# Optimization experiments

Measured on AMD Instinct MI355X. Metric: run time of the kernel, lower is better.

## Reference

```python
import jax, jax.numpy as jnp
import numpy as np

H = 4      # heads
C = 32     # out channels per head (hidden_channels)
G = 64     # num graphs


def transformer_conv(x, src, dst, Wq, bq, Wk, bk, Wv, bv, Ws, bs):
    # PyG TransformerConv, concat=False, root_weight=True, beta=False.
    N = x.shape[0]
    q = (x @ Wq + bq).reshape(N, H, C)
    k = (x @ Wk + bk).reshape(N, H, C)
    v = (x @ Wv + bv).reshape(N, H, C)
    qe = q[dst]            # [E,H,C] gather target queries
    ke = k[src]            # [E,H,C] gather source keys
    ve = v[src]            # [E,H,C] gather source values
    alpha = (qe * ke).sum(-1) / jnp.sqrt(jnp.asarray(C, x.dtype))  # [E,H]
    amax = jax.ops.segment_max(alpha, dst, num_segments=N)          # [N,H]
    a = jnp.exp(alpha - amax[dst])
    denom = jax.ops.segment_sum(a, dst, num_segments=N)             # [N,H]
    a = a / (denom[dst] + 1e-16)
    out = jax.ops.segment_sum(ve * a[..., None], dst, num_segments=N)  # [N,H,C]
    out = out.mean(axis=1)          # concat=False -> head average
    return out + x @ Ws + bs        # root skip


def setup_inputs() -> dict:
    key = jax.random.key(0)
    ks = jax.random.split(key, 24)
    N, E, Fin = 40000, 640000, 128
    x = jax.random.normal(ks[0], (N, Fin), dtype=jnp.float32)
    edge_index = jax.random.randint(ks[1], (2, E), 0, N, dtype=jnp.int64)
    batch = jnp.sort(jax.random.randint(ks[2], (N,), 0, G, dtype=jnp.int64))
    s = 0.05
    w = lambda k, shp: jax.random.normal(k, shp, dtype=jnp.float32) * s
    d = {"x": x, "edge_index": edge_index, "batch": batch,
         "Wq1": w(ks[3], (Fin, H * C)), "bq1": w(ks[4], (H * C,)),
         "Wk1": w(ks[5], (Fin, H * C)), "bk1": w(ks[6], (H * C,)),
         "Wv1": w(ks[7], (Fin, H * C)), "bv1": w(ks[8], (H * C,)),
         "Ws1": w(ks[9], (Fin, C)), "bs1": w(ks[10], (C,)),
         "Wq2": w(ks[11], (C, H * C)), "bq2": w(ks[12], (H * C,)),
         "Wk2": w(ks[13], (C, H * C)), "bk2": w(ks[14], (H * C,)),
         "Wv2": w(ks[15], (C, H * C)), "bv2": w(ks[16], (H * C,)),
         "Ws2": w(ks[17], (C, C)), "bs2": w(ks[18], (C,)),
         "Wlin": w(ks[19], (C, 16)), "blin": w(ks[20], (16,))}
    return d


def reference(x, edge_index, batch,
              Wq1, bq1, Wk1, bk1, Wv1, bv1, Ws1, bs1,
              Wq2, bq2, Wk2, bk2, Wv2, bv2, Ws2, bs2,
              Wlin, blin):
    src, dst = edge_index[0], edge_index[1]
    h = transformer_conv(x, src, dst, Wq1, bq1, Wk1, bk1, Wv1, bv1, Ws1, bs1)
    h = jax.nn.relu(h)
    h = transformer_conv(h, src, dst, Wq2, bq2, Wk2, bk2, Wv2, bv2, Ws2, bs2)
    # global mean pool over graphs
    sums = jax.ops.segment_sum(h, batch, num_segments=G)                  # [G,C]
    cnts = jax.ops.segment_sum(jnp.ones((h.shape[0],), h.dtype), batch, num_segments=G)
    pooled = sums / jnp.maximum(cnts, 1.0)[:, None]
    return pooled @ Wlin + blin
```

## Files before the change

### kernel.cpp

```cpp
#include <hip/hip_runtime.h>
#include <hip/hip_bf16.h>
#include <hip/hip_fp16.h>
#include <math.h>

#define HH 4
#define CC 32
#define HC 128
#define GG 64

typedef _Float16 f16x2 __attribute__((ext_vector_type(2)));
typedef _Float16 f16x8 __attribute__((ext_vector_type(8)));
typedef float f32x4 __attribute__((ext_vector_type(4)));

__device__ __forceinline__ f16x2 u2h(unsigned u) {
    union { unsigned u; f16x2 h; } x; x.u = u; return x.h;
}
__device__ __forceinline__ unsigned pkh(float a, float b) {
    __half2 h = __floats2half2_rn(a, b);
    union { __half2 h; unsigned u; } x; x.h = h; return x.u;
}
__device__ __forceinline__ f16x8 uq2h8(uint4 u) {
    union { uint4 u; f16x8 h; } x; x.u = u; return x.h;
}

__global__ void cvt_f2h_kernel(const float* __restrict__ in, unsigned* __restrict__ out, int n4)
{
    int i = blockIdx.x * 256 + threadIdx.x;
    if (i < n4) {
        float4 f = ((const float4*)in)[i];
        ((uint2*)out)[i] = make_uint2(pkh(f.x, f.y), pkh(f.z, f.w));
    }
}

__global__ void wfrag_kernel(const float* __restrict__ Wq, const float* __restrict__ Wk,
                             const float* __restrict__ Wv, const float* __restrict__ Ws,
                             uint4* __restrict__ wfrag, int KS)
{
    int idx = blockIdx.x * 256 + threadIdx.x;
    int total = 26 * KS * 64;
    if (idx >= total) return;
    int lane = idx & 63;
    int t = idx >> 6;
    int ks = t % KS, ct = t / KS;
    int r = lane & 15, g = lane >> 4;
    const float* W; int c, stride;
    if (ct < 8)       { W = Wq; c = ct * 16 + r;        stride = HC; }
    else if (ct < 16) { W = Wk; c = (ct - 8) * 16 + r;  stride = HC; }
    else if (ct < 24) { W = Wv; c = (ct - 16) * 16 + r; stride = HC; }
    else              { W = Ws; c = (ct - 24) * 16 + r; stride = CC; }
    unsigned u[4];
    #pragma unroll
    for (int jj = 0; jj < 4; ++jj) {
        int k = ks * 32 + g * 8 + jj * 2;
        u[jj] = pkh(W[(size_t)k * stride + c], W[(size_t)(k + 1) * stride + c]);
    }
    wfrag[idx] = make_uint4(u[0], u[1], u[2], u[3]);
}

template<int KDIM>
__global__ __launch_bounds__(256) void qkv_mfma_kernel(
    const ushort* __restrict__ xh, const uint4* __restrict__ wfrag,
    const float* __restrict__ bq, const float* __restrict__ bk,
    const float* __restrict__ bv, const float* __restrict__ bs,
    unsigned* __restrict__ qh, unsigned* __restrict__ kvw, float* __restrict__ skip,
    int N)
{
    constexpr int KS = KDIM / 32;
    const int lane = threadIdx.x & 63;
    const int wv = threadIdx.x >> 6;
    const int n0 = (blockIdx.x * 4 + wv) * 16;
    if (n0 >= N) return;
    const int r = lane & 15, g = lane >> 4;
    const int node = n0 + r;

    f16x8 a[KS];
    #pragma unroll
    for (int ks = 0; ks < KS; ++ks)
        a[ks] = uq2h8(*(const uint4*)&xh[(size_t)node * KDIM + ks * 32 + g * 8]);

    if (blockIdx.y == 0) {
        f32x4 acc[10];
        #pragma unroll
        for (int i = 0; i < 10; ++i) acc[i] = (f32x4){0.f, 0.f, 0.f, 0.f};
        #pragma unroll
        for (int i = 0; i < 8; ++i)
            #pragma unroll
            for (int ks = 0; ks < KS; ++ks) {
                f16x8 w = uq2h8(wfrag[((size_t)i * KS + ks) * 64 + lane]);
                acc[i] = __builtin_amdgcn_mfma_f32_16x16x32_f16(w, a[ks], acc[i], 0, 0, 0);
            }
        #pragma unroll
        for (int i = 0; i < 2; ++i)
            #pragma unroll
            for (int ks = 0; ks < KS; ++ks) {
                f16x8 w = uq2h8(wfrag[((size_t)(24 + i) * KS + ks) * 64 + lane]);
                acc[8 + i] = __builtin_amdgcn_mfma_f32_16x16x32_f16(w, a[ks], acc[8 + i], 0, 0, 0);
            }
        if (node < N) {
            #pragma unroll
            for (int i = 0; i < 8; ++i) {
                float4 bb = *(const float4*)&bq[i * 16 + g * 4];
                uint2 o = make_uint2(pkh(acc[i][0] + bb.x, acc[i][1] + bb.y),
                                     pkh(acc[i][2] + bb.z, acc[i][3] + bb.w));
                *(uint2*)&qh[(size_t)node * 64 + i * 8 + g * 2] = o;
            }
            #pragma unroll
            for (int i = 0; i < 2; ++i) {
                float4 bb = *(const float4*)&bs[i * 16 + g * 4];
                float4 o = make_float4(acc[8 + i][0] + bb.x, acc[8 + i][1] + bb.y,
                                       acc[8 + i][2] + bb.z, acc[8 + i][3] + bb.w);
                *(float4*)&skip[(size_t)node * CC + i * 16 + g * 4] = o;
            }
        }
    } else {
        f32x4 acck[8], accv[8];
        #pragma unroll
        for (int i = 0; i < 8; ++i) { acck[i] = (f32x4){0.f,0.f,0.f,0.f}; accv[i] = (f32x4){0.f,0.f,0.f,0.f}; }
        #pragma unroll
        for (int i = 0; i < 8; ++i)
            #pragma unroll
            for (int ks = 0; ks < KS; ++ks) {
                f16x8 wk = uq2h8(wfrag[((size_t)(8 + i) * KS + ks) * 64 + lane]);
                acck[i] = __builtin_amdgcn_mfma_f32_16x16x32_f16(wk, a[ks], acck[i], 0, 0, 0);
                f16x8 wvf = uq2h8(wfrag[((size_t)(16 + i) * KS + ks) * 64 + lane]);
                accv[i] = __builtin_amdgcn_mfma_f32_16x16x32_f16(wvf, a[ks], accv[i], 0, 0, 0);
            }
        if (node < N) {
            #pragma unroll
            for (int i = 0; i < 8; ++i) {
                float4 bbk = *(const float4*)&bk[i * 16 + g * 4];
                float4 bbv = *(const float4*)&bv[i * 16 + g * 4];
                uint4 o;
                o.x = pkh(acck[i][0] + bbk.x, acck[i][1] + bbk.y);
                o.y = pkh(accv[i][0] + bbv.x, accv[i][1] + bbv.y);
                o.z = pkh(acck[i][2] + bbk.z, acck[i][3] + bbk.w);
                o.w = pkh(accv[i][2] + bbv.z, accv[i][3] + bbv.w);
                *(uint4*)&kvw[(size_t)node * 128 + i * 16 + g * 4] = o;
            }
        }
    }
}

__global__ void deg_kernel(const int* __restrict__ dst, int* __restrict__ deg, int E)
{
    int e = blockIdx.x * blockDim.x + threadIdx.x;
    if (e < E) atomicAdd(&deg[dst[e]], 1);
}

__global__ void bsum_kernel(const int* __restrict__ deg, int* __restrict__ bsum, int N)
{
    int base = blockIdx.x * 1024;
    int tid = threadIdx.x;
    int s = 0;
    for (int i = base + tid; i < base + 1024 && i < N; i += 256) s += deg[i];
    #pragma unroll
    for (int ofs = 32; ofs > 0; ofs >>= 1) s += __shfl_xor(s, ofs, 64);
    __shared__ int ws[4];
    int wid = tid >> 6;
    if ((tid & 63) == 0) ws[wid] = s;
    __syncthreads();
    if (tid == 0) bsum[blockIdx.x] = ws[0] + ws[1] + ws[2] + ws[3];
}

__global__ void bscan_kernel(int* __restrict__ bsum, int* __restrict__ off, int nb, int N)
{
    int i = threadIdx.x;
    int val = (i < nb) ? bsum[i] : 0;
    int v = val;
    #pragma unroll
    for (int ofs = 1; ofs < 64; ofs <<= 1) {
        int t = __shfl_up(v, ofs, 64);
        if (i >= ofs) v += t;
    }
    if (i < nb) bsum[i] = v - val;
    if (i == 63) off[N] = v;
}

__global__ void scan2_kernel(const int* __restrict__ deg, const int* __restrict__ bsum,
                             int* __restrict__ off, int* __restrict__ cursor, int N)
{
    int base = blockIdx.x * 1024;
    int tid = threadIdx.x;
    int idx = base + tid * 4;
    int d0 = (idx     < N) ? deg[idx]     : 0;
    int d1 = (idx + 1 < N) ? deg[idx + 1] : 0;
    int d2 = (idx + 2 < N) ? deg[idx + 2] : 0;
    int d3 = (idx + 3 < N) ? deg[idx + 3] : 0;
    int tsum = d0 + d1 + d2 + d3;
    int v = tsum;
    int lane = tid & 63;
    #pragma unroll
    for (int ofs = 1; ofs < 64; ofs <<= 1) {
        int t = __shfl_up(v, ofs, 64);
        if (lane >= ofs) v += t;
    }
    __shared__ int wsum[4];
    int wid = tid >> 6;
    if (lane == 63) wsum[wid] = v;
    __syncthreads();
    int wbase = 0;
    for (int w = 0; w < wid; ++w) wbase += wsum[w];
    int excl = bsum[blockIdx.x] + wbase + (v - tsum);
    if (idx     < N) { off[idx]     = excl;                cursor[idx]     = excl; }
    if (idx + 1 < N) { off[idx + 1] = excl + d0;           cursor[idx + 1] = excl + d0; }
    if (idx + 2 < N) { off[idx + 2] = excl + d0 + d1;      cursor[idx + 2] = excl + d0 + d1; }
    if (idx + 3 < N) { off[idx + 3] = excl + d0 + d1 + d2; cursor[idx + 3] = excl + d0 + d1 + d2; }
}

__global__ void fill_kernel(const int* __restrict__ src, const int* __restrict__ dst,
                            int* __restrict__ cursor, int* __restrict__ esrc, int E)
{
    int e = blockIdx.x * blockDim.x + threadIdx.x;
    if (e < E) {
        int d = dst[e];
        int pos = atomicAdd(&cursor[d], 1);
        esrc[pos] = src[e];
    }
}

template<int MODE>
__global__ __launch_bounds__(128) void attn_kernel(const unsigned* __restrict__ qh,
    const uint2* __restrict__ kv2, const int* __restrict__ off, const int* __restrict__ esrc,
    const float* __restrict__ skip, void* __restrict__ hout, int N)
{
    const int wave = threadIdx.x >> 6;
    const int lane = threadIdx.x & 63;
    const int n = blockIdx.x * 2 + wave;
    if (n >= N) return;
    const int c2 = lane & 15;
    const float scale = 0.17677669529663687f;

    f16x2 q2 = u2h(qh[(size_t)n * 64 + lane]);
    int beg = __builtin_amdgcn_readfirstlane(off[n]);
    int end = __builtin_amdgcn_readfirstlane(off[n + 1]);

    float lsum = 0.f, ax = 0.f, ay = 0.f;

    auto body = [&](uint2 raw) {
        f16x2 k2 = u2h(raw.x), v2 = u2h(raw.y);
#if defined(__has_builtin) && __has_builtin(__builtin_amdgcn_fdot2)
        float d = __builtin_amdgcn_fdot2(q2, k2, 0.f, false);
#else
        float d = (float)q2.x * (float)k2.x + (float)q2.y * (float)k2.y;
#endif
        d += __shfl_xor(d, 1, 16);
        d += __shfl_xor(d, 2, 16);
        d += __shfl_xor(d, 4, 16);
        d += __shfl_xor(d, 8, 16);
        float e = __expf(d * scale);
        lsum += e;
        ax = fmaf(e, (float)v2.x, ax);
        ay = fmaf(e, (float)v2.y, ay);
    };

    int p = beg;
    for (; p + 4 <= end; p += 4) {
        int s0 = esrc[p], s1 = esrc[p + 1], s2 = esrc[p + 2], s3 = esrc[p + 3];
        uint2 r0 = kv2[(size_t)s0 * 64 + lane];
        uint2 r1 = kv2[(size_t)s1 * 64 + lane];
        uint2 r2 = kv2[(size_t)s2 * 64 + lane];
        uint2 r3 = kv2[(size_t)s3 * 64 + lane];
        body(r0); body(r1); body(r2); body(r3);
    }
    for (; p < end; ++p) {
        int s0 = esrc[p];
        body(kv2[(size_t)s0 * 64 + lane]);
    }

    float inv = 1.f / (lsum + 1e-16f);
    float rx = ax * inv, ry = ay * inv;
    rx += __shfl_xor(rx, 16, 64);  ry += __shfl_xor(ry, 16, 64);
    rx += __shfl_xor(rx, 32, 64);  ry += __shfl_xor(ry, 32, 64);
    if (lane < 16) {
        float2 sk = *(const float2*)&skip[(size_t)n * CC + c2 * 2];
        float ox = 0.25f * rx + sk.x;
        float oy = 0.25f * ry + sk.y;
        if (MODE) {
            ox = fmaxf(ox, 0.f); oy = fmaxf(oy, 0.f);
            ((unsigned*)hout)[(size_t)n * 16 + c2] = pkh(ox, oy);
        } else {
            *(float2*)&((float*)hout)[(size_t)n * CC + c2 * 2] = make_float2(ox, oy);
        }
    }
}

__global__ void pool_kernel(const float* __restrict__ h, const int* __restrict__ batch,
    float* __restrict__ sums, float* __restrict__ cntf, int N)
{
    int c = threadIdx.x & 31;
    int tn = threadIdx.x >> 5;
    int n0 = blockIdx.x * 256;
    int nend = (n0 + 256 < N) ? n0 + 256 : N;
    float acc = 0.f, cnt = 0.f;
    int curg = -1;
    for (int n = n0 + tn; n < nend; n += 8) {
        int g = batch[n];
        if (g != curg) {
            if (curg >= 0) {
                unsafeAtomicAdd(&sums[curg * CC + c], acc);
                if (c == 0) unsafeAtomicAdd(&cntf[curg], cnt);
            }
            acc = 0.f; cnt = 0.f; curg = g;
        }
        acc += h[(size_t)n * CC + c];
        cnt += 1.f;
    }
    if (curg >= 0) {
        unsafeAtomicAdd(&sums[curg * CC + c], acc);
        if (c == 0) unsafeAtomicAdd(&cntf[curg], cnt);
    }
}

__global__ void final_lin_kernel(const float* __restrict__ sums, const float* __restrict__ cntf,
    const float* __restrict__ Wlin, const float* __restrict__ blin, float* __restrict__ out)
{
    int g = blockIdx.x;
    int j = threadIdx.x;
    float cnt = fmaxf(cntf[g], 1.0f);
    float acc = 0.f;
    #pragma unroll
    for (int c = 0; c < CC; ++c)
        acc += (sums[g * CC + c] / cnt) * Wlin[c * 16 + j];
    out[g * 16 + j] = acc + blin[j];
}

extern "C" void kernel_launch(void* const* d_in, const int* in_sizes, int n_in,
                              void* d_out, int out_size, void* d_ws, size_t ws_size,
                              hipStream_t stream) {
    const float* x     = (const float*)d_in[0];
    const int*   ei    = (const int*)d_in[1];
    const int*   batch = (const int*)d_in[2];
    const float* Wq1 = (const float*)d_in[3],  *bq1 = (const float*)d_in[4];
    const float* Wk1 = (const float*)d_in[5],  *bk1 = (const float*)d_in[6];
    const float* Wv1 = (const float*)d_in[7],  *bv1 = (const float*)d_in[8];
    const float* Ws1 = (const float*)d_in[9],  *bs1 = (const float*)d_in[10];
    const float* Wq2 = (const float*)d_in[11], *bq2 = (const float*)d_in[12];
    const float* Wk2 = (const float*)d_in[13], *bk2 = (const float*)d_in[14];
    const float* Wv2 = (const float*)d_in[15], *bv2 = (const float*)d_in[16];
    const float* Ws2 = (const float*)d_in[17], *bs2 = (const float*)d_in[18];
    const float* Wlin = (const float*)d_in[19], *blin = (const float*)d_in[20];

    const int N = in_sizes[0] / 128;
    const int E = in_sizes[1] / 2;
    const int* src = ei;
    const int* dstp = ei + E;
    const int NB = (N + 1023) / 1024;
    const int Npad = (N + 63) & ~63;

    char* wp = (char*)d_ws;
    auto alloc = [&](size_t bytes) -> void* {
        void* p = wp;
        wp += (bytes + 255) & ~(size_t)255;
        return p;
    };
    unsigned* qh   = (unsigned*)alloc((size_t)N * 64 * 4);
    uint2* kv2     = (uint2*)alloc((size_t)N * 64 * 8);
    float* skip    = (float*)alloc((size_t)N * CC * 4);
    unsigned* h1h  = (unsigned*)alloc((size_t)Npad * 16 * 4);
    float* h2      = (float*)alloc((size_t)N * CC * 4);
    ushort* xh     = (ushort*)alloc((size_t)Npad * HC * 2);
    uint4* wfrag1  = (uint4*)alloc((size_t)26 * 4 * 64 * 16);
    uint4* wfrag2  = (uint4*)alloc((size_t)26 * 1 * 64 * 16);
    int* deg    = (int*)alloc((size_t)N * 4);
    int* off    = (int*)alloc((size_t)(N + 1) * 4);
    int* cursor = (int*)alloc((size_t)N * 4);
    int* esrc   = (int*)alloc((size_t)E * 4);
    int* bsum   = (int*)alloc((size_t)((NB + 63) & ~63) * 4);
    float* sums = (float*)alloc((size_t)GG * CC * 4);
    float* cntf = (float*)alloc((size_t)GG * 4);

    cvt_f2h_kernel<<<(N * HC / 4 + 255) / 256, 256, 0, stream>>>(x, (unsigned*)xh, N * HC / 4);
    wfrag_kernel<<<(26 * 4 * 64 + 255) / 256, 256, 0, stream>>>(Wq1, Wk1, Wv1, Ws1, wfrag1, 4);
    wfrag_kernel<<<(26 * 1 * 64 + 255) / 256, 256, 0, stream>>>(Wq2, Wk2, Wv2, Ws2, wfrag2, 1);

    hipMemsetAsync(deg, 0, (size_t)N * 4, stream);
    deg_kernel<<<(E + 255) / 256, 256, 0, stream>>>(dstp, deg, E);
    bsum_kernel<<<NB, 256, 0, stream>>>(deg, bsum, N);
    bscan_kernel<<<1, 64, 0, stream>>>(bsum, off, NB, N);
    scan2_kernel<<<NB, 256, 0, stream>>>(deg, bsum, off, cursor, N);
    fill_kernel<<<(E + 255) / 256, 256, 0, stream>>>(src, dstp, cursor, esrc, E);

    dim3 ggrid((N + 63) / 64, 2);
    dim3 agrid((N + 1) / 2);

    qkv_mfma_kernel<128><<<ggrid, 256, 0, stream>>>(xh, wfrag1, bq1, bk1, bv1, bs1,
                                                    qh, (unsigned*)kv2, skip, N);
    attn_kernel<1><<<agrid, 128, 0, stream>>>(qh, kv2, off, esrc, skip, h1h, N);

    qkv_mfma_kernel<32><<<ggrid, 256, 0, stream>>>((const ushort*)h1h, wfrag2, bq2, bk2, bv2, bs2,
                                                   qh, (unsigned*)kv2, skip, N);
    attn_kernel<0><<<agrid, 128, 0, stream>>>(qh, kv2, off, esrc, skip, h2, N);

    hipMemsetAsync(sums, 0, (size_t)GG * CC * 4, stream);
    hipMemsetAsync(cntf, 0, (size_t)GG * 4, stream);
    pool_kernel<<<(N + 255) / 256, 256, 0, stream>>>(h2, batch, sums, cntf, N);
    final_lin_kernel<<<GG, 16, 0, stream>>>(sums, cntf, Wlin, blin, (float*)d_out);
}
```

Measured before the change: 238.8 us.

## Repack KV for 128-bit gathers, process two edges per wave, fold softmax scale

```diff
diff --git a/kernel.cpp b/kernel.cpp
--- a/kernel.cpp
+++ b/kernel.cpp
@@ -32,13 +32,10 @@
     }
 }
 
-__global__ void wfrag_kernel(const float* __restrict__ Wq, const float* __restrict__ Wk,
-                             const float* __restrict__ Wv, const float* __restrict__ Ws,
-                             uint4* __restrict__ wfrag, int KS)
-{
-    int idx = blockIdx.x * 256 + threadIdx.x;
-    int total = 26 * KS * 64;
-    if (idx >= total) return;
+__device__ __forceinline__ void wfrag_item(const float* __restrict__ Wq, const float* __restrict__ Wk,
+    const float* __restrict__ Wv, const float* __restrict__ Ws,
+    uint4* __restrict__ wfrag, int KS, int idx)
+{
     int lane = idx & 63;
     int t = idx >> 6;
     int ks = t % KS, ct = t / KS;
@@ -57,12 +54,25 @@
     wfrag[idx] = make_uint4(u[0], u[1], u[2], u[3]);
 }
 
+__global__ void wfrag_both_kernel(
+    const float* __restrict__ Wq1, const float* __restrict__ Wk1,
+    const float* __restrict__ Wv1, const float* __restrict__ Ws1, uint4* __restrict__ wfrag1,
+    const float* __restrict__ Wq2, const float* __restrict__ Wk2,
+    const float* __restrict__ Wv2, const float* __restrict__ Ws2, uint4* __restrict__ wfrag2)
+{
+    int idx = blockIdx.x * 256 + threadIdx.x;
+    const int N1 = 26 * 4 * 64;
+    const int N2 = 26 * 1 * 64;
+    if (idx < N1) wfrag_item(Wq1, Wk1, Wv1, Ws1, wfrag1, 4, idx);
+    else if (idx < N1 + N2) wfrag_item(Wq2, Wk2, Wv2, Ws2, wfrag2, 1, idx - N1);
+}
+
 template<int KDIM>
 __global__ __launch_bounds__(256) void qkv_mfma_kernel(
     const ushort* __restrict__ xh, const uint4* __restrict__ wfrag,
     const float* __restrict__ bq, const float* __restrict__ bk,
     const float* __restrict__ bv, const float* __restrict__ bs,
-    unsigned* __restrict__ qh, unsigned* __restrict__ kvw, float* __restrict__ skip,
+    unsigned* __restrict__ qh, uint4* __restrict__ kv4, float* __restrict__ skip,
     int N)
 {
     constexpr int KS = KDIM / 32;
@@ -79,6 +89,7 @@
         a[ks] = uq2h8(*(const uint4*)&xh[(size_t)node * KDIM + ks * 32 + g * 8]);
 
     if (blockIdx.y == 0) {
+        const float SC2 = 0.25500526806584186f;
         f32x4 acc[10];
         #pragma unroll
         for (int i = 0; i < 10; ++i) acc[i] = (f32x4){0.f, 0.f, 0.f, 0.f};
@@ -100,8 +111,8 @@
             #pragma unroll
             for (int i = 0; i < 8; ++i) {
                 float4 bb = *(const float4*)&bq[i * 16 + g * 4];
-                uint2 o = make_uint2(pkh(acc[i][0] + bb.x, acc[i][1] + bb.y),
-                                     pkh(acc[i][2] + bb.z, acc[i][3] + bb.w));
+                uint2 o = make_uint2(pkh((acc[i][0] + bb.x) * SC2, (acc[i][1] + bb.y) * SC2),
+                                     pkh((acc[i][2] + bb.z) * SC2, (acc[i][3] + bb.w) * SC2));
                 *(uint2*)&qh[(size_t)node * 64 + i * 8 + g * 2] = o;
             }
             #pragma unroll
@@ -132,10 +143,10 @@
                 float4 bbv = *(const float4*)&bv[i * 16 + g * 4];
                 uint4 o;
                 o.x = pkh(acck[i][0] + bbk.x, acck[i][1] + bbk.y);
-                o.y = pkh(accv[i][0] + bbv.x, accv[i][1] + bbv.y);
-                o.z = pkh(acck[i][2] + bbk.z, acck[i][3] + bbk.w);
+                o.y = pkh(acck[i][2] + bbk.z, acck[i][3] + bbk.w);
+                o.z = pkh(accv[i][0] + bbv.x, accv[i][1] + bbv.y);
                 o.w = pkh(accv[i][2] + bbv.z, accv[i][3] + bbv.w);
-                *(uint4*)&kvw[(size_t)node * 128 + i * 16 + g * 4] = o;
+                kv4[(size_t)node * 32 + i * 4 + g] = o;
             }
         }
     }
@@ -220,66 +231,85 @@
 
 template<int MODE>
 __global__ __launch_bounds__(128) void attn_kernel(const unsigned* __restrict__ qh,
-    const uint2* __restrict__ kv2, const int* __restrict__ off, const int* __restrict__ esrc,
+    const uint4* __restrict__ kv4, const int* __restrict__ off, const int* __restrict__ esrc,
     const float* __restrict__ skip, void* __restrict__ hout, int N)
 {
     const int wave = threadIdx.x >> 6;
     const int lane = threadIdx.x & 63;
     const int n = blockIdx.x * 2 + wave;
     if (n >= N) return;
-    const int c2 = lane & 15;
-    const float scale = 0.17677669529663687f;
-
-    f16x2 q2 = u2h(qh[(size_t)n * 64 + lane]);
+    const int half = lane >> 5;
+    const int j = lane & 31;
+
+    uint2 qv = *(const uint2*)&qh[(size_t)n * 64 + j * 2];
+    f16x2 q01 = u2h(qv.x), q23 = u2h(qv.y);
+
     int beg = __builtin_amdgcn_readfirstlane(off[n]);
     int end = __builtin_amdgcn_readfirstlane(off[n + 1]);
 
-    float lsum = 0.f, ax = 0.f, ay = 0.f;
-
-    auto body = [&](uint2 raw) {
-        f16x2 k2 = u2h(raw.x), v2 = u2h(raw.y);
+    float lsum = 0.f, a0 = 0.f, a1 = 0.f, a2 = 0.f, a3 = 0.f;
+
+    auto body = [&](int idx, bool guard) {
+        int sidx = (guard && idx >= end) ? end - 1 : idx;
+        int s = esrc[sidx];
+        uint4 raw = kv4[(size_t)s * 32 + j];
+        f16x2 k01 = u2h(raw.x), k23 = u2h(raw.y);
+        f16x2 v01 = u2h(raw.z), v23 = u2h(raw.w);
 #if defined(__has_builtin) && __has_builtin(__builtin_amdgcn_fdot2)
-        float d = __builtin_amdgcn_fdot2(q2, k2, 0.f, false);
+        float d = __builtin_amdgcn_fdot2(q01, k01,
+                    __builtin_amdgcn_fdot2(q23, k23, 0.f, false), false);
 #else
-        float d = (float)q2.x * (float)k2.x + (float)q2.y * (float)k2.y;
+        float d = (float)q01.x*(float)k01.x + (float)q01.y*(float)k01.y
+                + (float)q23.x*(float)k23.x + (float)q23.y*(float)k23.y;
 #endif
-        d += __shfl_xor(d, 1, 16);
-        d += __shfl_xor(d, 2, 16);
-        d += __shfl_xor(d, 4, 16);
-        d += __shfl_xor(d, 8, 16);
-        float e = __expf(d * scale);
+        d += __shfl_xor(d, 1, 8);
+        d += __shfl_xor(d, 2, 8);
+        d += __shfl_xor(d, 4, 8);
+        float e = exp2f(d);
+        if (guard && idx >= end) e = 0.f;
         lsum += e;
-        ax = fmaf(e, (float)v2.x, ax);
-        ay = fmaf(e, (float)v2.y, ay);
+        a0 = fmaf(e, (float)v01.x, a0);
+        a1 = fmaf(e, (float)v01.y, a1);
+        a2 = fmaf(e, (float)v23.x, a2);
+        a3 = fmaf(e, (float)v23.y, a3);
     };
 
     int p = beg;
-    for (; p + 4 <= end; p += 4) {
-        int s0 = esrc[p], s1 = esrc[p + 1], s2 = esrc[p + 2], s3 = esrc[p + 3];
-        uint2 r0 = kv2[(size_t)s0 * 64 + lane];
-        uint2 r1 = kv2[(size_t)s1 * 64 + lane];
-        uint2 r2 = kv2[(size_t)s2 * 64 + lane];
-        uint2 r3 = kv2[(size_t)s3 * 64 + lane];
-        body(r0); body(r1); body(r2); body(r3);
-    }
-    for (; p < end; ++p) {
-        int s0 = esrc[p];
-        body(kv2[(size_t)s0 * 64 + lane]);
-    }
+    for (; p + 8 <= end; p += 8) {
+        body(p + half, false);
+        body(p + 2 + half, false);
+        body(p + 4 + half, false);
+        body(p + 6 + half, false);
+    }
+    for (; p < end; p += 2) body(p + half, true);
+
+    lsum += __shfl_xor(lsum, 32);
+    a0 += __shfl_xor(a0, 32);
+    a1 += __shfl_xor(a1, 32);
+    a2 += __shfl_xor(a2, 32);
+    a3 += __shfl_xor(a3, 32);
 
     float inv = 1.f / (lsum + 1e-16f);
-    float rx = ax * inv, ry = ay * inv;
-    rx += __shfl_xor(rx, 16, 64);  ry += __shfl_xor(ry, 16, 64);
-    rx += __shfl_xor(rx, 32, 64);  ry += __shfl_xor(ry, 32, 64);
-    if (lane < 16) {
-        float2 sk = *(const float2*)&skip[(size_t)n * CC + c2 * 2];
-        float ox = 0.25f * rx + sk.x;
-        float oy = 0.25f * ry + sk.y;
+    float r0 = a0 * inv, r1 = a1 * inv, r2 = a2 * inv, r3 = a3 * inv;
+    r0 += __shfl_xor(r0, 8, 32);  r0 += __shfl_xor(r0, 16, 32);
+    r1 += __shfl_xor(r1, 8, 32);  r1 += __shfl_xor(r1, 16, 32);
+    r2 += __shfl_xor(r2, 8, 32);  r2 += __shfl_xor(r2, 16, 32);
+    r3 += __shfl_xor(r3, 8, 32);  r3 += __shfl_xor(r3, 16, 32);
+
+    if (lane < 8) {
+        float4 sk = *(const float4*)&skip[(size_t)n * CC + lane * 4];
+        float o0 = 0.25f * r0 + sk.x;
+        float o1 = 0.25f * r1 + sk.y;
+        float o2 = 0.25f * r2 + sk.z;
+        float o3 = 0.25f * r3 + sk.w;
         if (MODE) {
-            ox = fmaxf(ox, 0.f); oy = fmaxf(oy, 0.f);
-            ((unsigned*)hout)[(size_t)n * 16 + c2] = pkh(ox, oy);
+            o0 = fmaxf(o0, 0.f); o1 = fmaxf(o1, 0.f);
+            o2 = fmaxf(o2, 0.f); o3 = fmaxf(o3, 0.f);
+            *(uint2*)&((unsigned*)hout)[(size_t)n * 16 + lane * 2] =
+                make_uint2(pkh(o0, o1), pkh(o2, o3));
         } else {
-            *(float2*)&((float*)hout)[(size_t)n * CC + c2 * 2] = make_float2(ox, oy);
+            *(float4*)&((float*)hout)[(size_t)n * CC + lane * 4] =
+                make_float4(o0, o1, o2, o3);
         }
     }
 }
@@ -354,7 +384,7 @@
         return p;
     };
     unsigned* qh   = (unsigned*)alloc((size_t)N * 64 * 4);
-    uint2* kv2     = (uint2*)alloc((size_t)N * 64 * 8);
+    uint4* kv4     = (uint4*)alloc((size_t)N * 32 * 16);
     float* skip    = (float*)alloc((size_t)N * CC * 4);
     unsigned* h1h  = (unsigned*)alloc((size_t)Npad * 16 * 4);
     float* h2      = (float*)alloc((size_t)N * CC * 4);
@@ -370,8 +400,8 @@
     float* cntf = (float*)alloc((size_t)GG * 4);
 
     cvt_f2h_kernel<<<(N * HC / 4 + 255) / 256, 256, 0, stream>>>(x, (unsigned*)xh, N * HC / 4);
-    wfrag_kernel<<<(26 * 4 * 64 + 255) / 256, 256, 0, stream>>>(Wq1, Wk1, Wv1, Ws1, wfrag1, 4);
-    wfrag_kernel<<<(26 * 1 * 64 + 255) / 256, 256, 0, stream>>>(Wq2, Wk2, Wv2, Ws2, wfrag2, 1);
+    wfrag_both_kernel<<<(26 * 5 * 64 + 255) / 256, 256, 0, stream>>>(
+        Wq1, Wk1, Wv1, Ws1, wfrag1, Wq2, Wk2, Wv2, Ws2, wfrag2);
 
     hipMemsetAsync(deg, 0, (size_t)N * 4, stream);
     deg_kernel<<<(E + 255) / 256, 256, 0, stream>>>(dstp, deg, E);
@@ -384,15 +414,14 @@
     dim3 agrid((N + 1) / 2);
 
     qkv_mfma_kernel<128><<<ggrid, 256, 0, stream>>>(xh, wfrag1, bq1, bk1, bv1, bs1,
-                                                    qh, (unsigned*)kv2, skip, N);
-    attn_kernel<1><<<agrid, 128, 0, stream>>>(qh, kv2, off, esrc, skip, h1h, N);
+                                                    qh, kv4, skip, N);
+    attn_kernel<1><<<agrid, 128, 0, stream>>>(qh, kv4, off, esrc, skip, h1h, N);
 
     qkv_mfma_kernel<32><<<ggrid, 256, 0, stream>>>((const ushort*)h1h, wfrag2, bq2, bk2, bv2, bs2,
-                                                   qh, (unsigned*)kv2, skip, N);
-    attn_kernel<0><<<agrid, 128, 0, stream>>>(qh, kv2, off, esrc, skip, h2, N);
-
-    hipMemsetAsync(sums, 0, (size_t)GG * CC * 4, stream);
-    hipMemsetAsync(cntf, 0, (size_t)GG * 4, stream);
+                                                   qh, kv4, skip, N);
+    attn_kernel<0><<<agrid, 128, 0, stream>>>(qh, kv4, off, esrc, skip, h2, N);
+
+    hipMemsetAsync(sums, 0, (size_t)(GG * CC + GG) * 4, stream);
     pool_kernel<<<(N + 255) / 256, 256, 0, stream>>>(h2, batch, sums, cntf, N);
     final_lin_kernel<<<GG, 16, 0, stream>>>(sums, cntf, Wlin, blin, (float*)d_out);
 }
```

Result: no change. 238.9 us (+0.0%).
